# Kernel optimization log

Measured on AMD Instinct MI355X. Metric: run time of the kernel, lower is better.

The kernel has to match this reference:

```python
import jax, jax.numpy as jnp
import numpy as np

N_NODES = 100000
N_EDGES = 640000
C_IN = 128
C_OUT = 128
E_DIM = 64
LN_EPS = 1e-5


def setup_inputs() -> dict:
    key = jax.random.key(0)
    ks = jax.random.split(key, 10)
    x = jax.random.normal(ks[0], (N_NODES, C_IN), dtype=jnp.float32)
    edge_index = jax.random.randint(ks[1], (2, N_EDGES), 0, N_NODES, dtype=jnp.int32)
    edge_attr = jax.random.normal(ks[2], (N_EDGES, E_DIM), dtype=jnp.float32)
    # lin_edge: edge_dim -> in_channels
    We = jax.random.normal(ks[3], (E_DIM, C_IN), dtype=jnp.float32) / np.sqrt(E_DIM)
    be = jnp.zeros((C_IN,), dtype=jnp.float32)
    # mlp: Linear(C, 2C) -> LayerNorm(2C) -> ReLU -> Linear(2C, C_OUT)
    W1 = jax.random.normal(ks[4], (C_IN, 2 * C_IN), dtype=jnp.float32) / np.sqrt(C_IN)
    b1 = jnp.zeros((2 * C_IN,), dtype=jnp.float32)
    gamma = jnp.ones((2 * C_IN,), dtype=jnp.float32)
    beta = jnp.zeros((2 * C_IN,), dtype=jnp.float32)
    W2 = jax.random.normal(ks[5], (2 * C_IN, C_OUT), dtype=jnp.float32) / np.sqrt(2 * C_IN)
    b2 = jnp.zeros((C_OUT,), dtype=jnp.float32)
    eps = jnp.zeros((1,), dtype=jnp.float32)  # learnable GIN epsilon, init 0
    return {"x": x, "edge_index": edge_index, "edge_attr": edge_attr,
            "We": We, "be": be, "W1": W1, "b1": b1, "gamma": gamma,
            "beta": beta, "W2": W2, "b2": b2, "eps": eps}


def reference(x, edge_index, edge_attr, We, be, W1, b1, gamma, beta, W2, b2, eps):
    # edge feature projection: [E, E_DIM] @ [E_DIM, C] -> [E, C]
    real_edge_attr = edge_attr @ We + be
    # gather source-node features (edge_index[1]), add edge features, relu
    message = jax.nn.relu(x[edge_index[1]] + real_edge_attr)  # [E, C]
    # scatter-add to destination nodes (edge_index[0])
    message_reduce = jax.ops.segment_sum(message, edge_index[0], num_segments=x.shape[0])
    h = (1.0 + eps) * x + message_reduce  # [N, C]
    # MLP: Linear -> LayerNorm -> ReLU -> Linear
    h1 = h @ W1 + b1  # [N, 2C]
    mu = jnp.mean(h1, axis=-1, keepdims=True)
    var = jnp.mean(jnp.square(h1 - mu), axis=-1, keepdims=True)
    h1 = (h1 - mu) * jax.lax.rsqrt(var + LN_EPS) * gamma + beta
    h1 = jax.nn.relu(h1)
    return h1 @ W2 + b2  # [N, C_OUT]
```

## Files before the change

### kernel.cpp

```cpp
#include <hip/hip_runtime.h>
#include <hip/hip_bf16.h>
#include <stdint.h>

#define NNODES 100000
#define NEDGES 640000
#define CIN 128
#define EDIM 64
#define C2 256
#define LN_EPS 1e-5f
#define NW 6144
#define PP 105
#define NB 391

typedef __attribute__((ext_vector_type(8))) short bf16x8;
typedef __attribute__((ext_vector_type(4))) float f32x4;

__device__ __forceinline__ ushort f2bf(float f) {
    uint32_t u = __float_as_uint(f);
    uint32_t r = (u + 0x7fffu + ((u >> 16) & 1u)) >> 16;
    return (ushort)r;
}
__device__ __forceinline__ uint32_t pack2(float a, float b) {
    return (uint32_t)f2bf(a) | ((uint32_t)f2bf(b) << 16);
}
__device__ __forceinline__ float bf2f_lo(uint32_t u) { return __uint_as_float(u << 16); }
__device__ __forceinline__ float bf2f_hi(uint32_t u) { return __uint_as_float(u & 0xffff0000u); }

union U16 { uint4 u; bf16x8 v; };

__global__ __launch_bounds__(256) void k_prep(
    const float* __restrict__ x, const float* __restrict__ W1,
    const float* __restrict__ W2, uint32_t* __restrict__ xbf,
    ushort* __restrict__ W1T, ushort* __restrict__ W2T,
    int* __restrict__ cursor)
{
    const int bid = blockIdx.x;
    if (bid < 6250) {
        const int i = bid * 256 + threadIdx.x;
        const float4* xg = (const float4*)x;
        const float4 v0 = xg[i * 2];
        const float4 v1 = xg[i * 2 + 1];
        uint4 o;
        o.x = pack2(v0.x, v0.y); o.y = pack2(v0.z, v0.w);
        o.z = pack2(v1.x, v1.y); o.w = pack2(v1.z, v1.w);
        ((uint4*)xbf)[i] = o;
    } else if (bid < 6506) {
        const int idx = (bid - 6250) * 256 + threadIdx.x;
        if (idx < 32768) {
            const int k = idx >> 8, c = idx & 255;
            W1T[c * 128 + k] = f2bf(W1[idx]);
        } else {
            const int j = idx - 32768;
            const int k = j >> 7, c = j & 127;
            W2T[c * 256 + k] = f2bf(W2[j]);
        }
    } else {
        const int n = (bid - 6506) * 256 + threadIdx.x;
        if (n < NNODES) cursor[n] = 0;
    }
}

__global__ __launch_bounds__(256) void k_hist(const int* __restrict__ ei,
                                              int* __restrict__ counts)
{
    const int e = blockIdx.x * 256 + threadIdx.x;
    atomicAdd(&counts[ei[e]], 1);
}

__global__ __launch_bounds__(256) void k_sA(const int* __restrict__ counts,
                                            int* __restrict__ bsum)
{
    const int t = threadIdx.x, lane = t & 63, wv = t >> 6;
    const int i = blockIdx.x * 256 + t;
    int s = (i < NNODES) ? counts[i] : 0;
#pragma unroll
    for (int off = 1; off < 64; off <<= 1) s += __shfl_xor(s, off);
    __shared__ int ws[4];
    if (lane == 0) ws[wv] = s;
    __syncthreads();
    if (t == 0) bsum[blockIdx.x] = ws[0] + ws[1] + ws[2] + ws[3];
}

__global__ __launch_bounds__(512) void k_sB(int* __restrict__ bsum)
{
    const int t = threadIdx.x, lane = t & 63, wv = t >> 6;
    const int v = (t < NB) ? bsum[t] : 0;
    int s = v;
#pragma unroll
    for (int off = 1; off < 64; off <<= 1) {
        const int u = __shfl_up(s, off);
        if (lane >= off) s += u;
    }
    __shared__ int ws[8];
    if (lane == 63) ws[wv] = s;
    __syncthreads();
    int off0 = 0;
    for (int w = 0; w < wv; ++w) off0 += ws[w];
    if (t < NB) bsum[t] = off0 + s - v;
}

__global__ __launch_bounds__(256) void k_sC(const int* __restrict__ bsum,
                                            int* __restrict__ cursor,
                                            int* __restrict__ rowptr)
{
    const int t = threadIdx.x, lane = t & 63, wv = t >> 6;
    const int i = blockIdx.x * 256 + t;
    const int v = (i < NNODES) ? cursor[i] : 0;
    int s = v;
#pragma unroll
    for (int off = 1; off < 64; off <<= 1) {
        const int u = __shfl_up(s, off);
        if (lane >= off) s += u;
    }
    __shared__ int ws[4];
    if (lane == 63) ws[wv] = s;
    __syncthreads();
    int off0 = bsum[blockIdx.x];
    for (int w = 0; w < wv; ++w) off0 += ws[w];
    const int excl = off0 + s - v;
    if (i < NNODES) { rowptr[i] = excl; cursor[i] = excl; }
    if (i == NNODES - 1) rowptr[NNODES] = excl + v;
}

__global__ __launch_bounds__(256) void k_fillp(const int* __restrict__ ei,
                                               int* __restrict__ cursor,
                                               int4* __restrict__ efs,
                                               const int* __restrict__ rowptr,
                                               int* __restrict__ naw,
                                               uint32_t* __restrict__ hbf)
{
    const int bid = blockIdx.x;
    if (bid < 2500) {
        const int e = bid * 256 + threadIdx.x;
        const int d = ei[e];
        const int pos = atomicAdd(&cursor[d], 1);
        int4 rec; rec.x = e; rec.y = ei[NEDGES + e]; rec.z = d; rec.w = 0;
        efs[pos] = rec;
    } else if (bid < 2525) {
        const int w = (bid - 2500) * 256 + threadIdx.x;
        if (w > NW) return;
        if (w == NW) { naw[w] = NNODES; return; }
        const int target = min(w * PP, NEDGES);
        int lo = 0, hi = NNODES;
        while (lo < hi) {
            const int mid = (lo + hi) >> 1;
            if (rowptr[mid] < target) lo = mid + 1; else hi = mid;
        }
        naw[w] = lo;
    } else {
        const int n = (bid - 2525) * 256 + threadIdx.x;
        if (n < NNODES && rowptr[n] == rowptr[n + 1]) {
            uint32_t* r = hbf + (size_t)n * 64;
#pragma unroll
            for (int i = 0; i < 64; ++i) r[i] = 0;
        }
    }
}

__global__ __launch_bounds__(256, 3) void k_edge(
    const uint32_t* __restrict__ xbf, const float* __restrict__ ea,
    const float* __restrict__ We, const float* __restrict__ be,
    const int4* __restrict__ efs, const int* __restrict__ naw,
    const int* __restrict__ rowptr, uint32_t* __restrict__ hbf)
{
    __shared__ float msgl[4 * 16 * 128];
    const int tid = threadIdx.x;
    const int l = tid & 63, q = l >> 4, m16 = l & 15;
    const int wv = tid >> 6;
    const int w = blockIdx.x * 4 + wv;

    bf16x8 bfw[2][8];
#pragma unroll
    for (int ks = 0; ks < 2; ++ks)
#pragma unroll
        for (int t = 0; t < 8; ++t) {
            const int c = m16 + 16 * t;
#pragma unroll
            for (int j = 0; j < 8; ++j)
                bfw[ks][t][j] = (short)f2bf(We[(ks * 32 + q * 8 + j) * CIN + c]);
        }
    const float2 bev = ((const float2*)be)[l];

    const int n0 = naw[w], n1 = naw[w + 1];
    const int ps = rowptr[n0], pe = rowptr[n1];
    char* msb = (char*)msgl + wv * 8192;
    const int pmax = NEDGES - 1;

    int cur = -1;
    float a0 = 0.f, a1 = 0.f;

    for (int ts = ps; ts < pe; ts += 16) {
        const int nt = min(16, pe - ts);
        const int pp = min(ts + m16, pmax);
        const int4 rec = efs[pp];
        const int ep = rec.x, sb = rec.y, db = rec.z;

        const float* ar = ea + (size_t)ep * EDIM + q * 8;
        const float4 f0 = *(const float4*)ar;
        const float4 f1 = *(const float4*)(ar + 4);
        const float4 g0 = *(const float4*)(ar + 32);
        const float4 g1 = *(const float4*)(ar + 36);

        uint xr[16];
#pragma unroll
        for (int jj = 0; jj < 16; ++jj) {
            const int sj = __builtin_amdgcn_readlane(sb, jj);
            if (jj < nt) xr[jj] = xbf[(size_t)sj * 64 + l];
        }

        bf16x8 A0, A1;
        A0[0] = (short)f2bf(f0.x); A0[1] = (short)f2bf(f0.y);
        A0[2] = (short)f2bf(f0.z); A0[3] = (short)f2bf(f0.w);
        A0[4] = (short)f2bf(f1.x); A0[5] = (short)f2bf(f1.y);
        A0[6] = (short)f2bf(f1.z); A0[7] = (short)f2bf(f1.w);
        A1[0] = (short)f2bf(g0.x); A1[1] = (short)f2bf(g0.y);
        A1[2] = (short)f2bf(g0.z); A1[3] = (short)f2bf(g0.w);
        A1[4] = (short)f2bf(g1.x); A1[5] = (short)f2bf(g1.y);
        A1[6] = (short)f2bf(g1.z); A1[7] = (short)f2bf(g1.w);

#pragma unroll
        for (int hf = 0; hf < 2; ++hf) {
            f32x4 acc4[4];
#pragma unroll
            for (int t4 = 0; t4 < 4; ++t4) acc4[t4] = (f32x4){0.f, 0.f, 0.f, 0.f};
#pragma unroll
            for (int t4 = 0; t4 < 4; ++t4) {
                acc4[t4] = __builtin_amdgcn_mfma_f32_16x16x32_bf16(A0, bfw[0][hf * 4 + t4], acc4[t4], 0, 0, 0);
                acc4[t4] = __builtin_amdgcn_mfma_f32_16x16x32_bf16(A1, bfw[1][hf * 4 + t4], acc4[t4], 0, 0, 0);
            }
#pragma unroll
            for (int t4 = 0; t4 < 4; ++t4) {
                const int col = m16 + 16 * (hf * 4 + t4);
#pragma unroll
                for (int r = 0; r < 4; ++r) {
                    const int row = q * 4 + r;
                    *(float*)(msb + row * 512 + ((4 * col) ^ ((row & 7) << 4))) = acc4[t4][r];
                }
            }
        }

#pragma unroll
        for (int jj = 0; jj < 16; ++jj) {
            if (jj < nt) {
                const int dj = __builtin_amdgcn_readlane(db, jj);
                if (dj != cur) {
                    if (cur >= 0)
                        hbf[(size_t)cur * 64 + l] = pack2(a0, a1);
                    cur = dj; a0 = 0.f; a1 = 0.f;
                }
                const uint32_t xu = xr[jj];
                const float2 mv = *(const float2*)(msb + jj * 512 + ((8 * l) ^ ((jj & 7) << 4)));
                a0 += fmaxf(bf2f_lo(xu) + mv.x + bev.x, 0.f);
                a1 += fmaxf(bf2f_hi(xu) + mv.y + bev.y, 0.f);
            }
        }
    }
    if (cur >= 0)
        hbf[(size_t)cur * 64 + l] = pack2(a0, a1);
}

__global__ __launch_bounds__(512, 4) void k23_fused(
    const uint32_t* __restrict__ hbf, const uint32_t* __restrict__ xbf,
    const float* __restrict__ eps, const ushort* __restrict__ W1T,
    const ushort* __restrict__ W2T, const float* __restrict__ b1,
    const float* __restrict__ gamma, const float* __restrict__ beta,
    const float* __restrict__ b2, float* __restrict__ out)
{
    __shared__ ushort w1t[CIN * C2];

    const int tid = threadIdx.x;
    {
        const uint4* w1g = (const uint4*)W1T;
#pragma unroll
        for (int i = tid; i < 4096; i += 512) {
            const int c = i >> 4, inb = (i & 15) << 4;
            *(uint4*)((char*)w1t + c * 256 + (inb ^ ((c & 15) << 4))) = w1g[i];
        }
    }
    const float s1p = 1.0f + eps[0];
    __syncthreads();

    const int l = tid & 63, q = l >> 4, m16 = l & 15;
    const int w = tid >> 6;
    const int n0 = blockIdx.x * 128 + w * 16;
    const int rowA = min(n0 + m16, NNODES - 1);

    f32x4 acc[16];
#pragma unroll
    for (int t = 0; t < 16; ++t) acc[t] = (f32x4){0.f, 0.f, 0.f, 0.f};

    const char* w1b = (const char*)w1t;
#pragma unroll
    for (int ks = 0; ks < 4; ++ks) {
        const uint4 su = *(const uint4*)(hbf + (size_t)rowA * 64 + ks * 16 + q * 4);
        const uint4 xu = *(const uint4*)(xbf + (size_t)rowA * 64 + ks * 16 + q * 4);
        U16 A;
        A.v[0] = (short)f2bf(fmaf(s1p, bf2f_lo(xu.x), bf2f_lo(su.x)));
        A.v[1] = (short)f2bf(fmaf(s1p, bf2f_hi(xu.x), bf2f_hi(su.x)));
        A.v[2] = (short)f2bf(fmaf(s1p, bf2f_lo(xu.y), bf2f_lo(su.y)));
        A.v[3] = (short)f2bf(fmaf(s1p, bf2f_hi(xu.y), bf2f_hi(su.y)));
        A.v[4] = (short)f2bf(fmaf(s1p, bf2f_lo(xu.z), bf2f_lo(su.z)));
        A.v[5] = (short)f2bf(fmaf(s1p, bf2f_hi(xu.z), bf2f_hi(su.z)));
        A.v[6] = (short)f2bf(fmaf(s1p, bf2f_lo(xu.w), bf2f_lo(su.w)));
        A.v[7] = (short)f2bf(fmaf(s1p, bf2f_hi(xu.w), bf2f_hi(su.w)));
        const int inrow = (ks * 64 + q * 16) ^ (m16 << 4);
#pragma unroll
        for (int t = 0; t < 16; ++t) {
            U16 B; B.u = *(const uint4*)(w1b + (size_t)(m16 + 16 * t) * 256 + inrow);
            acc[t] = __builtin_amdgcn_mfma_f32_16x16x32_bf16(A.v, B.v, acc[t], 0, 0, 0);
        }
    }

    float s[4] = {0.f, 0.f, 0.f, 0.f}, sq[4] = {0.f, 0.f, 0.f, 0.f};
#pragma unroll
    for (int t = 0; t < 16; ++t) {
        const float bb = b1[m16 + 16 * t];
#pragma unroll
        for (int r = 0; r < 4; ++r) {
            acc[t][r] += bb;
            s[r]  += acc[t][r];
            sq[r] += acc[t][r] * acc[t][r];
        }
    }
#pragma unroll
    for (int off = 1; off < 16; off <<= 1)
#pragma unroll
        for (int r = 0; r < 4; ++r) {
            s[r]  += __shfl_xor(s[r],  off);
            sq[r] += __shfl_xor(sq[r], off);
        }
    float mu[4], is[4];
#pragma unroll
    for (int r = 0; r < 4; ++r) {
        mu[r] = s[r] * (1.0f / 256.0f);
        const float var = sq[r] * (1.0f / 256.0f) - mu[r] * mu[r];
        is[r] = rsqrtf(var + LN_EPS);
    }

    __syncthreads();

    char* hls = (char*)w1t + w * 8192;
#pragma unroll
    for (int t = 0; t < 16; ++t) {
        const int c = m16 + 16 * t;
        const float g = gamma[c], b = beta[c];
#pragma unroll
        for (int r = 0; r < 4; ++r) {
            const int row = q * 4 + r;
            const float o = fmaxf((acc[t][r] - mu[r]) * is[r] * g + b, 0.0f);
            *(ushort*)(hls + row * 512 + ((2 * c) ^ (row << 4))) = f2bf(o);
        }
    }
    __syncthreads();

    f32x4 acc2[8];
#pragma unroll
    for (int t = 0; t < 8; ++t) acc2[t] = (f32x4){0.f, 0.f, 0.f, 0.f};

    const char* w2g = (const char*)W2T;
#pragma unroll
    for (int ks = 0; ks < 8; ++ks) {
        const int inrow = (ks * 64 + q * 16) ^ (m16 << 4);
        const int inrow2 = ks * 64 + q * 16;
        U16 A; A.u = *(const uint4*)(hls + m16 * 512 + inrow);
#pragma unroll
        for (int t = 0; t < 8; ++t) {
            U16 B; B.u = *(const uint4*)(w2g + (size_t)(m16 + 16 * t) * 512 + inrow2);
            acc2[t] = __builtin_amdgcn_mfma_f32_16x16x32_bf16(A.v, B.v, acc2[t], 0, 0, 0);
        }
    }
#pragma unroll
    for (int t = 0; t < 8; ++t) {
        const int c = m16 + 16 * t;
        const float bb = b2[c];
#pragma unroll
        for (int r = 0; r < 4; ++r) {
            const int row = n0 + q * 4 + r;
            if (row < NNODES)
                out[(size_t)row * CIN + c] = acc2[t][r] + bb;
        }
    }
}

extern "C" void kernel_launch(void* const* d_in, const int* in_sizes, int n_in,
                              void* d_out, int out_size, void* d_ws, size_t ws_size,
                              hipStream_t stream)
{
    const float* x     = (const float*)d_in[0];
    const int*   ei    = (const int*)d_in[1];
    const float* ea    = (const float*)d_in[2];
    const float* We    = (const float*)d_in[3];
    const float* be    = (const float*)d_in[4];
    const float* W1    = (const float*)d_in[5];
    const float* b1    = (const float*)d_in[6];
    const float* gamma = (const float*)d_in[7];
    const float* beta  = (const float*)d_in[8];
    const float* W2    = (const float*)d_in[9];
    const float* b2    = (const float*)d_in[10];
    const float* eps   = (const float*)d_in[11];

    char* wsB = (char*)d_ws;
    uint32_t* hbf   = (uint32_t*)wsB;
    int*      rowptr= (int*)(wsB + 25600000);
    int*      cursor= (int*)(wsB + 26001408);
    int4*     efs   = (int4*)(wsB + 26401408);
    int*      naw   = (int*)(wsB + 36641408);
    int*      bsum  = (int*)(wsB + 36666368);
    uint32_t* xbf   = (uint32_t*)(wsB + 36668416);
    ushort*   W1T   = (ushort*)(wsB + 62268416);
    ushort*   W2T   = (ushort*)(wsB + 62333952);

    k_prep <<<6897, 256, 0, stream>>>(x, W1, W2, xbf, W1T, W2T, cursor);
    k_hist <<<NEDGES / 256, 256, 0, stream>>>(ei, cursor);
    k_sA   <<<NB, 256, 0, stream>>>(cursor, bsum);
    k_sB   <<<1, 512, 0, stream>>>(bsum);
    k_sC   <<<NB, 256, 0, stream>>>(bsum, cursor, rowptr);
    k_fillp<<<2916, 256, 0, stream>>>(ei, cursor, efs, rowptr, naw, hbf);

    k_edge <<<NW / 4, 256, 0, stream>>>(xbf, ea, We, be, efs, naw,
                                        rowptr, hbf);

    k23_fused<<<(NNODES + 127) / 128, 512, 0, stream>>>(hbf, xbf, eps, W1T, W2T,
                                                        b1, gamma, beta, b2,
                                                        (float*)d_out);
}
```

Baseline: 249.7 us.

## Merge scan kernels, store edge messages as bf16 in LDS, fewer edge waves

```diff
diff --git a/kernel.cpp b/kernel.cpp
--- a/kernel.cpp
+++ b/kernel.cpp
@@ -8,8 +8,8 @@
 #define EDIM 64
 #define C2 256
 #define LN_EPS 1e-5f
-#define NW 6144
-#define PP 105
+#define NW 4096
+#define PP 157
 #define NB 391
 
 typedef __attribute__((ext_vector_type(8))) short bf16x8;
@@ -81,41 +81,33 @@
     if (t == 0) bsum[blockIdx.x] = ws[0] + ws[1] + ws[2] + ws[3];
 }
 
-__global__ __launch_bounds__(512) void k_sB(int* __restrict__ bsum)
-{
+__global__ __launch_bounds__(256) void k_sC(const int* __restrict__ bsum,
+                                            int* __restrict__ cursor,
+                                            int* __restrict__ rowptr)
+{
+    __shared__ int wred[4];
+    __shared__ int ws[4];
     const int t = threadIdx.x, lane = t & 63, wv = t >> 6;
-    const int v = (t < NB) ? bsum[t] : 0;
+
+    int part = 0;
+    for (int j = t; j < blockIdx.x; j += 256) part += bsum[j];
+#pragma unroll
+    for (int off = 1; off < 64; off <<= 1) part += __shfl_xor(part, off);
+    if (lane == 0) wred[wv] = part;
+    __syncthreads();
+    const int blockoff = wred[0] + wred[1] + wred[2] + wred[3];
+
+    const int i = blockIdx.x * 256 + t;
+    const int v = (i < NNODES) ? cursor[i] : 0;
     int s = v;
 #pragma unroll
     for (int off = 1; off < 64; off <<= 1) {
         const int u = __shfl_up(s, off);
         if (lane >= off) s += u;
     }
-    __shared__ int ws[8];
     if (lane == 63) ws[wv] = s;
     __syncthreads();
-    int off0 = 0;
-    for (int w = 0; w < wv; ++w) off0 += ws[w];
-    if (t < NB) bsum[t] = off0 + s - v;
-}
-
-__global__ __launch_bounds__(256) void k_sC(const int* __restrict__ bsum,
-                                            int* __restrict__ cursor,
-                                            int* __restrict__ rowptr)
-{
-    const int t = threadIdx.x, lane = t & 63, wv = t >> 6;
-    const int i = blockIdx.x * 256 + t;
-    const int v = (i < NNODES) ? cursor[i] : 0;
-    int s = v;
-#pragma unroll
-    for (int off = 1; off < 64; off <<= 1) {
-        const int u = __shfl_up(s, off);
-        if (lane >= off) s += u;
-    }
-    __shared__ int ws[4];
-    if (lane == 63) ws[wv] = s;
-    __syncthreads();
-    int off0 = bsum[blockIdx.x];
+    int off0 = blockoff;
     for (int w = 0; w < wv; ++w) off0 += ws[w];
     const int excl = off0 + s - v;
     if (i < NNODES) { rowptr[i] = excl; cursor[i] = excl; }
@@ -136,7 +128,7 @@
         const int pos = atomicAdd(&cursor[d], 1);
         int4 rec; rec.x = e; rec.y = ei[NEDGES + e]; rec.z = d; rec.w = 0;
         efs[pos] = rec;
-    } else if (bid < 2525) {
+    } else if (bid < 2517) {
         const int w = (bid - 2500) * 256 + threadIdx.x;
         if (w > NW) return;
         if (w == NW) { naw[w] = NNODES; return; }
@@ -148,7 +140,7 @@
         }
         naw[w] = lo;
     } else {
-        const int n = (bid - 2525) * 256 + threadIdx.x;
+        const int n = (bid - 2517) * 256 + threadIdx.x;
         if (n < NNODES && rowptr[n] == rowptr[n + 1]) {
             uint32_t* r = hbf + (size_t)n * 64;
 #pragma unroll
@@ -163,7 +155,7 @@
     const int4* __restrict__ efs, const int* __restrict__ naw,
     const int* __restrict__ rowptr, uint32_t* __restrict__ hbf)
 {
-    __shared__ float msgl[4 * 16 * 128];
+    __shared__ uint32_t msgl[4 * 16 * 64];
     const int tid = threadIdx.x;
     const int l = tid & 63, q = l >> 4, m16 = l & 15;
     const int wv = tid >> 6;
@@ -183,7 +175,7 @@
 
     const int n0 = naw[w], n1 = naw[w + 1];
     const int ps = rowptr[n0], pe = rowptr[n1];
-    char* msb = (char*)msgl + wv * 8192;
+    char* msb = (char*)msgl + wv * 4096;
     const int pmax = NEDGES - 1;
 
     int cur = -1;
@@ -234,7 +226,7 @@
 #pragma unroll
                 for (int r = 0; r < 4; ++r) {
                     const int row = q * 4 + r;
-                    *(float*)(msb + row * 512 + ((4 * col) ^ ((row & 7) << 4))) = acc4[t4][r];
+                    *(ushort*)(msb + row * 256 + ((2 * col) ^ (row << 4))) = f2bf(acc4[t4][r]);
                 }
             }
         }
@@ -249,9 +241,9 @@
                     cur = dj; a0 = 0.f; a1 = 0.f;
                 }
                 const uint32_t xu = xr[jj];
-                const float2 mv = *(const float2*)(msb + jj * 512 + ((8 * l) ^ ((jj & 7) << 4)));
-                a0 += fmaxf(bf2f_lo(xu) + mv.x + bev.x, 0.f);
-                a1 += fmaxf(bf2f_hi(xu) + mv.y + bev.y, 0.f);
+                const uint32_t mv = *(const uint32_t*)(msb + jj * 256 + ((4 * l) ^ (jj << 4)));
+                a0 += fmaxf(bf2f_lo(xu) + bf2f_lo(mv) + bev.x, 0.f);
+                a1 += fmaxf(bf2f_hi(xu) + bf2f_hi(mv) + bev.y, 0.f);
             }
         }
     }
@@ -413,9 +405,8 @@
     k_prep <<<6897, 256, 0, stream>>>(x, W1, W2, xbf, W1T, W2T, cursor);
     k_hist <<<NEDGES / 256, 256, 0, stream>>>(ei, cursor);
     k_sA   <<<NB, 256, 0, stream>>>(cursor, bsum);
-    k_sB   <<<1, 512, 0, stream>>>(bsum);
     k_sC   <<<NB, 256, 0, stream>>>(bsum, cursor, rowptr);
-    k_fillp<<<2916, 256, 0, stream>>>(ei, cursor, efs, rowptr, naw, hbf);
+    k_fillp<<<2908, 256, 0, stream>>>(ei, cursor, efs, rowptr, naw, hbf);
 
     k_edge <<<NW / 4, 256, 0, stream>>>(xbf, ea, We, be, efs, naw,
                                         rowptr, hbf);
```

Measured after the change: 300.4 us. 1.2x slower.
